# Performance work log

Measured on AMD Instinct MI355X. Metric: run time of the kernel, lower is better.

Reference implementation:

```python
import jax, jax.numpy as jnp
import numpy as np

N_NODES = 100000
IN_CH = 128
HID = 256
EMB = 128
N_EDGES_GRAPH = 1000000
N_PAIRS = 500000
BN_EPS = 1e-5


def setup_inputs() -> dict:
    key = jax.random.key(0)
    ks = jax.random.split(key, 20)
    glorot = lambda k, fi, fo: jax.random.normal(k, (fi, fo), jnp.float32) * (1.0 / np.sqrt(fi))
    pair_dim = EMB * 4 + 2  # 514
    return {
        "x": jax.random.normal(ks[0], (N_NODES, IN_CH), jnp.float32),
        "edge_index": jax.random.randint(ks[1], (2, N_EDGES_GRAPH), 0, N_NODES, jnp.int64),
        "edge_pairs": jax.random.randint(ks[2], (N_PAIRS, 2), 0, N_NODES, jnp.int64),
        # normalizer buffers
        "x_mean": jnp.zeros((IN_CH,), jnp.float32),
        "x_std": jnp.ones((IN_CH,), jnp.float32),
        # log-degree buffer (as after set_degree)
        "log_degree": jax.random.uniform(ks[3], (N_NODES,), jnp.float32) * 5.0,
        # encoder: Linear(in,hid) -> BN(hid) -> ReLU -> Dropout -> Linear(hid,emb) -> ReLU
        "W1": glorot(ks[4], IN_CH, HID), "b1": jnp.zeros((HID,), jnp.float32),
        "bn_gamma": jnp.ones((HID,), jnp.float32), "bn_beta": jnp.zeros((HID,), jnp.float32),
        "bn_mean": jnp.zeros((HID,), jnp.float32), "bn_var": jnp.ones((HID,), jnp.float32),
        "W2": glorot(ks[5], HID, EMB), "b2": jnp.zeros((EMB,), jnp.float32),
        # scorer: Linear(514,256) -> ReLU -> Dropout -> Linear(256,128) -> ReLU -> Linear(128,1)
        "SW1": glorot(ks[6], pair_dim, HID), "Sb1": jnp.zeros((HID,), jnp.float32),
        "SW2": glorot(ks[7], HID, HID // 2), "Sb2": jnp.zeros((HID // 2,), jnp.float32),
        "SW3": glorot(ks[8], HID // 2, 1), "Sb3": jnp.zeros((1,), jnp.float32),
    }


def reference(x, edge_index, edge_pairs, x_mean, x_std, log_degree,
              W1, b1, bn_gamma, bn_beta, bn_mean, bn_var, W2, b2,
              SW1, Sb1, SW2, Sb2, SW3, Sb3):
    # ---- encode ----
    xf = jnp.nan_to_num(x, nan=0.0, posinf=0.0, neginf=0.0)
    xf = jnp.clip((xf - x_mean) / x_std, -10.0, 10.0)
    h = xf @ W1 + b1                                    # [N, HID]
    h = (h - bn_mean) * jax.lax.rsqrt(bn_var + BN_EPS) * bn_gamma + bn_beta  # BN (eval)
    h = jax.nn.relu(h)                                  # dropout = identity (eval)
    z = jax.nn.relu(h @ W2 + b2)                        # [N, EMB]
    # ---- score_from_embeddings ----
    si = edge_pairs[:, 0]
    di = edge_pairs[:, 1]
    src = z[si]                                         # [E, EMB]
    dst = z[di]
    deg_pair = jnp.stack([log_degree[si], log_degree[di]], axis=1)  # [E, 2]
    pair = jnp.concatenate([src, dst, src * dst, jnp.abs(src - dst), deg_pair], axis=1)  # [E, 4*EMB+2]
    s = jax.nn.relu(pair @ SW1 + Sb1)
    s = jax.nn.relu(s @ SW2 + Sb2)
    logits = (s @ SW3 + Sb3).reshape(-1)                # [E]
    return jnp.nan_to_num(logits, nan=0.0, posinf=20.0, neginf=-20.0)
```

## Files before the change

kernel.cpp:

```cpp
#include <hip/hip_runtime.h>
#include <hip/hip_bf16.h>
#include <math.h>

typedef unsigned short u16;
typedef __attribute__((ext_vector_type(8))) short bf16x8;
typedef __attribute__((ext_vector_type(8))) unsigned short u16x8;
typedef __attribute__((ext_vector_type(4))) float f32x4;
typedef __attribute__((ext_vector_type(4))) unsigned u32x4;
typedef __attribute__((ext_vector_type(2))) unsigned u32x2;

#define N_NODES 100000
#define IN_CH 128
#define HID 256
#define EMB 128
#define N_PAIRS 500000
#define BN_EPS 1e-5f

#define PBM 64

__device__ __forceinline__ u16 f2bf(float f) {
    unsigned u = __builtin_bit_cast(unsigned, f);
    unsigned r = u + 0x7FFFu + ((u >> 16) & 1u);
    return (u16)(r >> 16);
}
__device__ __forceinline__ float bf2f(u16 h) {
    unsigned u = ((unsigned)h) << 16;
    return __builtin_bit_cast(float, u);
}
__device__ __forceinline__ unsigned pk2(float a, float b) {
    __hip_bfloat162 h = __float22bfloat162_rn(make_float2(a, b));
    unsigned u;
    __builtin_memcpy(&u, &h, sizeof(u));
    return u;
}
__device__ __forceinline__ float lo16f(unsigned u) { return __builtin_bit_cast(float, u << 16); }
__device__ __forceinline__ float hi16f(unsigned u) { return __builtin_bit_cast(float, u & 0xffff0000u); }

__device__ __forceinline__ void store8(u16* buf, int base, const float* v) {
    u32x4 hv;
    #pragma unroll
    for (int q = 0; q < 4; ++q) hv[q] = pk2(v[2 * q], v[2 * q + 1]);
    *reinterpret_cast<u32x4*>(&buf[base]) = hv;
}

__global__ __launch_bounds__(256) void prep_weights(
    const float* __restrict__ SW1, const float* __restrict__ SW2,
    const float* __restrict__ W1,  const float* __restrict__ W2,
    u16* __restrict__ w1h, u16* __restrict__ w2h,
    u16* __restrict__ w1nh, u16* __restrict__ w1nl,
    u16* __restrict__ w2nh, u16* __restrict__ w2nl)
{
    const int tid = blockIdx.x * 256 + threadIdx.x;
    if (tid < 131072) {
        const int j = tid & 7, l = (tid >> 3) & 63, ks = (tid >> 9) & 15, mt = tid >> 13;
        const int n = mt * 16 + (l & 15);
        const int k = ks * 32 + ((l >> 4) << 3) + j;
        w1h[tid] = f2bf(SW1[(size_t)k * HID + n]);
    } else if (tid < 163840) {
        const int t2 = tid - 131072;
        const int j = t2 & 7, l = (t2 >> 3) & 63, ks = (t2 >> 9) & 7, mt = t2 >> 12;
        const int n = mt * 16 + (l & 15);
        const int k = ks * 32 + ((l >> 4) << 3) + j;
        w2h[t2] = f2bf(SW2[(size_t)k * (HID / 2) + n]);
    } else if (tid < 196608) {
        const int t3 = tid - 163840;
        const int j = t3 & 7, l = (t3 >> 3) & 63, ks = (t3 >> 9) & 3, mt = t3 >> 11;
        const int n = mt * 16 + (l & 15);
        const int k = ks * 32 + ((l >> 4) << 3) + j;
        const float v = W1[(size_t)k * HID + n];
        const u16 h = f2bf(v);
        w1nh[t3] = h;
        w1nl[t3] = f2bf(v - bf2f(h));
    } else if (tid < 229376) {
        const int t4 = tid - 196608;
        const int j = t4 & 7, l = (t4 >> 3) & 63, ks = (t4 >> 9) & 7, mt = t4 >> 12;
        const int n = mt * 16 + (l & 15);
        const int k = ks * 32 + ((l >> 4) << 3) + j;
        const float v = W2[(size_t)k * EMB + n];
        const u16 h = f2bf(v);
        w2nh[t4] = h;
        w2nl[t4] = f2bf(v - bf2f(h));
    }
}

__global__ __launch_bounds__(256) void node_mfma_kernel(
    const float* __restrict__ x,
    const float* __restrict__ x_mean, const float* __restrict__ x_std,
    const float* __restrict__ b1,
    const float* __restrict__ bn_gamma, const float* __restrict__ bn_beta,
    const float* __restrict__ bn_mean,  const float* __restrict__ bn_var,
    const float* __restrict__ b2,
    const u16* __restrict__ w1nh, const u16* __restrict__ w1nl,
    const u16* __restrict__ w2nh, const u16* __restrict__ w2nl,
    u16* __restrict__ z)
{
    __shared__ __align__(16) u16 XF[8192];
    __shared__ __align__(16) u16 HF[16384];

    const int t   = threadIdx.x;
    const int w   = t >> 6;
    const int l   = t & 63;
    const int l15 = l & 15;
    const int l4  = l >> 4;
    const int n0  = blockIdx.x * 64;
    const int nd  = (n0 + l < N_NODES) ? (n0 + l) : (N_NODES - 1);

    {
        const float* xp = x + (size_t)nd * IN_CH + w * 32;
        float v[32];
        #pragma unroll
        for (int q = 0; q < 8; ++q)
            *reinterpret_cast<float4*>(&v[q * 4]) = *reinterpret_cast<const float4*>(xp + q * 4);
        #pragma unroll
        for (int q = 0; q < 8; ++q) {
            float4 m4 = *reinterpret_cast<const float4*>(x_mean + w * 32 + q * 4);
            float4 s4 = *reinterpret_cast<const float4*>(x_std  + w * 32 + q * 4);
            float mm[4] = {m4.x, m4.y, m4.z, m4.w};
            float ss[4] = {s4.x, s4.y, s4.z, s4.w};
            #pragma unroll
            for (int e = 0; e < 4; ++e) {
                float val = v[q * 4 + e];
                if (!isfinite(val)) val = 0.0f;
                val = (val - mm[e]) / ss[e];
                v[q * 4 + e] = fminf(fmaxf(val, -10.0f), 10.0f);
            }
        }
        #pragma unroll
        for (int q = 0; q < 4; ++q) {
            const int base = (w * 4 + l4) * 512 + (l15 + 16 * q) * 8;
            store8(XF, base, &v[q * 8]);
        }
    }
    __syncthreads();

    f32x4 acc[4][4];
    #pragma unroll
    for (int m = 0; m < 4; ++m)
        #pragma unroll
        for (int nt = 0; nt < 4; ++nt) acc[m][nt] = (f32x4){0.f, 0.f, 0.f, 0.f};

    #pragma unroll
    for (int sl = 0; sl < 4; ++sl) {
        bf16x8 wh[4], wl[4];
        #pragma unroll
        for (int m = 0; m < 4; ++m) {
            const size_t bo = ((size_t)((w * 4 + m) * 4 + sl) * 64 + l) * 8;
            wh[m] = *reinterpret_cast<const bf16x8*>(&w1nh[bo]);
            wl[m] = *reinterpret_cast<const bf16x8*>(&w1nl[bo]);
        }
        bf16x8 fh[4];
        #pragma unroll
        for (int nt = 0; nt < 4; ++nt)
            fh[nt] = *reinterpret_cast<const bf16x8*>(&XF[(sl * 4 + nt) * 512 + l * 8]);
        __builtin_amdgcn_s_setprio(1);
        #pragma unroll
        for (int m = 0; m < 4; ++m)
            #pragma unroll
            for (int nt = 0; nt < 4; ++nt)
                acc[m][nt] = __builtin_amdgcn_mfma_f32_16x16x32_bf16(wh[m], fh[nt], acc[m][nt], 0, 0, 0);
        #pragma unroll
        for (int m = 0; m < 4; ++m)
            #pragma unroll
            for (int nt = 0; nt < 4; ++nt)
                acc[m][nt] = __builtin_amdgcn_mfma_f32_16x16x32_bf16(wl[m], fh[nt], acc[m][nt], 0, 0, 0);
        __builtin_amdgcn_s_setprio(0);
    }

    #pragma unroll
    for (int m = 0; m < 4; ++m) {
        const int mt = w * 4 + m;
        const int nb = mt * 16 + l4 * 4;
        float4 b1v = *reinterpret_cast<const float4*>(b1 + nb);
        float4 gv  = *reinterpret_cast<const float4*>(bn_gamma + nb);
        float4 bev = *reinterpret_cast<const float4*>(bn_beta + nb);
        float4 mev = *reinterpret_cast<const float4*>(bn_mean + nb);
        float4 vav = *reinterpret_cast<const float4*>(bn_var + nb);
        float scale[4], shift[4];
        float bb[4] = {b1v.x, b1v.y, b1v.z, b1v.w};
        float gg[4] = {gv.x, gv.y, gv.z, gv.w};
        float be[4] = {bev.x, bev.y, bev.z, bev.w};
        float me[4] = {mev.x, mev.y, mev.z, mev.w};
        float va[4] = {vav.x, vav.y, vav.z, vav.w};
        #pragma unroll
        for (int r = 0; r < 4; ++r) {
            scale[r] = gg[r] * rsqrtf(va[r] + BN_EPS);
            shift[r] = (bb[r] - me[r]) * scale[r] + be[r];
        }
        #pragma unroll
        for (int nt = 0; nt < 4; ++nt) {
            float v[4];
            #pragma unroll
            for (int r = 0; r < 4; ++r)
                v[r] = fmaxf(fmaf(acc[m][nt][r], scale[r], shift[r]), 0.0f);
            u32x2 hv;
            hv[0] = pk2(v[0], v[1]);
            hv[1] = pk2(v[2], v[3]);
            const int base = ((mt >> 1) * 4 + nt) * 512
                           + (l15 + 16 * ((mt & 1) * 2 + (l4 >> 1))) * 8
                           + (l4 & 1) * 4;
            *reinterpret_cast<u32x2*>(&HF[base]) = hv;
        }
    }
    __syncthreads();

    f32x4 acc2[2][4];
    #pragma unroll
    for (int m2 = 0; m2 < 2; ++m2)
        #pragma unroll
        for (int nt = 0; nt < 4; ++nt) acc2[m2][nt] = (f32x4){0.f, 0.f, 0.f, 0.f};

    #pragma unroll
    for (int ks2 = 0; ks2 < 8; ++ks2) {
        bf16x8 wh2[2], wl2[2];
        #pragma unroll
        for (int m2 = 0; m2 < 2; ++m2) {
            const size_t bo = ((size_t)((w * 2 + m2) * 8 + ks2) * 64 + l) * 8;
            wh2[m2] = *reinterpret_cast<const bf16x8*>(&w2nh[bo]);
            wl2[m2] = *reinterpret_cast<const bf16x8*>(&w2nl[bo]);
        }
        bf16x8 fh[4];
        #pragma unroll
        for (int nt = 0; nt < 4; ++nt)
            fh[nt] = *reinterpret_cast<const bf16x8*>(&HF[(ks2 * 4 + nt) * 512 + l * 8]);
        __builtin_amdgcn_s_setprio(1);
        #pragma unroll
        for (int m2 = 0; m2 < 2; ++m2)
            #pragma unroll
            for (int nt = 0; nt < 4; ++nt)
                acc2[m2][nt] = __builtin_amdgcn_mfma_f32_16x16x32_bf16(wh2[m2], fh[nt], acc2[m2][nt], 0, 0, 0);
        #pragma unroll
        for (int m2 = 0; m2 < 2; ++m2)
            #pragma unroll
            for (int nt = 0; nt < 4; ++nt)
                acc2[m2][nt] = __builtin_amdgcn_mfma_f32_16x16x32_bf16(wl2[m2], fh[nt], acc2[m2][nt], 0, 0, 0);
        __builtin_amdgcn_s_setprio(0);
    }

    #pragma unroll
    for (int m2 = 0; m2 < 2; ++m2) {
        const int nb2 = (w * 2 + m2) * 16 + l4 * 4;
        float4 b2v = *reinterpret_cast<const float4*>(b2 + nb2);
        float bb[4] = {b2v.x, b2v.y, b2v.z, b2v.w};
        #pragma unroll
        for (int nt = 0; nt < 4; ++nt) {
            const int node = n0 + nt * 16 + l15;
            if (node < N_NODES) {
                float v0 = fmaxf(acc2[m2][nt][0] + bb[0], 0.0f);
                float v1 = fmaxf(acc2[m2][nt][1] + bb[1], 0.0f);
                float v2 = fmaxf(acc2[m2][nt][2] + bb[2], 0.0f);
                float v3 = fmaxf(acc2[m2][nt][3] + bb[3], 0.0f);
                u32x2 hv;
                hv[0] = pk2(v0, v1);
                hv[1] = pk2(v2, v3);
                *reinterpret_cast<u32x2*>(z + (size_t)node * EMB + nb2) = hv;
            }
        }
    }
}

__global__ __launch_bounds__(256) void pair_mfma_kernel(
    const u16* __restrict__ z,
    const int* __restrict__ pairs,
    const float* __restrict__ logdeg,
    const u16* __restrict__ w1h,
    const u16* __restrict__ w2h,
    const float* __restrict__ SW1, const float* __restrict__ Sb1,
    const float* __restrict__ Sb2,
    const float* __restrict__ SW3, const float* __restrict__ Sb3,
    float* __restrict__ out)
{
    __shared__ __align__(16) u16 Abuf[8192];
    __shared__ __align__(16) u16 Bbuf[8192];
    __shared__ float red[4][4][16];

    const int t   = threadIdx.x;
    const int w   = t >> 6;
    const int l   = t & 63;
    const int l15 = l & 15;
    const int l4  = l >> 4;
    const int p0  = blockIdx.x * PBM;

    const int qb  = (w & 1) * 2;
    const int bS0 = (((w >> 1)) * 4 + l4) * 512 + (l15 + 16 * (qb + 0)) * 8;
    const int bS1 = (((w >> 1)) * 4 + l4) * 512 + (l15 + 16 * (qb + 1)) * 8;
    const int bD0 = ((2 + (w >> 1)) * 4 + l4) * 512 + (l15 + 16 * (qb + 0)) * 8;
    const int bD1 = ((2 + (w >> 1)) * 4 + l4) * 512 + (l15 + 16 * (qb + 1)) * 8;

    const int gp  = (p0 + l < N_PAIRS) ? (p0 + l) : (N_PAIRS - 1);
    const int gsi = pairs[(size_t)gp * 2 + 0];
    const int gdi = pairs[(size_t)gp * 2 + 1];

    const u16* zs0 = z + (size_t)gsi * EMB + w * 16;
    const u16* zd0 = z + (size_t)gdi * EMB + w * 16;
    u16x8 s00 = *reinterpret_cast<const u16x8*>(zs0);
    u16x8 s01 = *reinterpret_cast<const u16x8*>(zs0 + 8);
    u16x8 d00 = *reinterpret_cast<const u16x8*>(zd0);
    u16x8 d01 = *reinterpret_cast<const u16x8*>(zd0 + 8);
    u16x8 s10 = *reinterpret_cast<const u16x8*>(zs0 + 64);
    u16x8 s11 = *reinterpret_cast<const u16x8*>(zs0 + 72);
    u16x8 d10 = *reinterpret_cast<const u16x8*>(zd0 + 64);
    u16x8 d11 = *reinterpret_cast<const u16x8*>(zd0 + 72);

    *reinterpret_cast<u16x8*>(&Abuf[bS0]) = s00;
    *reinterpret_cast<u16x8*>(&Abuf[bS1]) = s01;
    *reinterpret_cast<u16x8*>(&Abuf[bD0]) = d00;
    *reinterpret_cast<u16x8*>(&Abuf[bD1]) = d01;

    float ldS[4], ldD[4];
    #pragma unroll
    for (int nt = 0; nt < 4; ++nt) {
        const int pidx = (p0 + nt * 16 + l15 < N_PAIRS) ? (p0 + nt * 16 + l15) : (N_PAIRS - 1);
        ldS[nt] = logdeg[pairs[(size_t)pidx * 2 + 0]];
        ldD[nt] = logdeg[pairs[(size_t)pidx * 2 + 1]];
    }

    __syncthreads();

    f32x4 acc[4][4];
    #pragma unroll
    for (int m = 0; m < 4; ++m)
        #pragma unroll
        for (int nt = 0; nt < 4; ++nt) acc[m][nt] = (f32x4){0.f, 0.f, 0.f, 0.f};

    auto run_pass = [&](const u16* buf, int k0, int k1, int k2, int k3) {
        const int ksg[4] = {k0, k1, k2, k3};
        bf16x8 wh[2][4];
        #pragma unroll
        for (int m = 0; m < 4; ++m) {
            const size_t bo = ((size_t)((w * 4 + m) * 16 + ksg[0]) * 64 + l) * 8;
            wh[0][m] = *reinterpret_cast<const bf16x8*>(&w1h[bo]);
        }
        #pragma unroll
        for (int sl = 0; sl < 4; ++sl) {
            const int cur = sl & 1;
            if (sl < 3) {
                #pragma unroll
                for (int m = 0; m < 4; ++m) {
                    const size_t bo = ((size_t)((w * 4 + m) * 16 + ksg[sl + 1]) * 64 + l) * 8;
                    wh[cur ^ 1][m] = *reinterpret_cast<const bf16x8*>(&w1h[bo]);
                }
            }
            #pragma unroll
            for (int nh = 0; nh < 2; ++nh) {
                bf16x8 fh[2];
                #pragma unroll
                for (int e = 0; e < 2; ++e)
                    fh[e] = *reinterpret_cast<const bf16x8*>(&buf[(sl * 4 + nh * 2 + e) * 512 + l * 8]);
                __builtin_amdgcn_s_setprio(1);
                #pragma unroll
                for (int m = 0; m < 4; ++m)
                    #pragma unroll
                    for (int e = 0; e < 2; ++e)
                        acc[m][nh * 2 + e] = __builtin_amdgcn_mfma_f32_16x16x32_bf16(wh[cur][m], fh[e], acc[m][nh * 2 + e], 0, 0, 0);
                __builtin_amdgcn_s_setprio(0);
            }
        }
    };

    auto rebuildR = [&](u16x8 sa, u16x8 sb, u16x8 da, u16x8 db, float* pv, float* av) {
        #pragma unroll
        for (int qq = 0; qq < 8; ++qq) {
            const float s = bf2f(sa[qq]);
            const float d = bf2f(da[qq]);
            pv[qq] = s * d;
            av[qq] = fabsf(s - d);
        }
        #pragma unroll
        for (int qq = 0; qq < 8; ++qq) {
            const float s = bf2f(sb[qq]);
            const float d = bf2f(db[qq]);
            pv[8 + qq] = s * d;
            av[8 + qq] = fabsf(s - d);
        }
    };

    run_pass(Abuf, 0, 1, 4, 5);
    {
        float pv[16], av[16];
        rebuildR(s00, s01, d00, d01, pv, av);
        store8(Bbuf, bS0, pv + 0);
        store8(Bbuf, bS1, pv + 8);
        store8(Bbuf, bD0, av + 0);
        store8(Bbuf, bD1, av + 8);
    }
    __syncthreads();

    *reinterpret_cast<u16x8*>(&Abuf[bS0]) = s10;
    *reinterpret_cast<u16x8*>(&Abuf[bS1]) = s11;
    *reinterpret_cast<u16x8*>(&Abuf[bD0]) = d10;
    *reinterpret_cast<u16x8*>(&Abuf[bD1]) = d11;
    run_pass(Bbuf, 8, 9, 12, 13);
    __syncthreads();

    run_pass(Abuf, 2, 3, 6, 7);
    {
        float pv[16], av[16];
        rebuildR(s10, s11, d10, d11, pv, av);
        store8(Bbuf, bS0, pv + 0);
        store8(Bbuf, bS1, pv + 8);
        store8(Bbuf, bD0, av + 0);
        store8(Bbuf, bD1, av + 8);
    }
    __syncthreads();

    run_pass(Bbuf, 10, 11, 14, 15);

    f32x4 acc2[2][4];
    #pragma unroll
    for (int m2 = 0; m2 < 2; ++m2)
        #pragma unroll
        for (int nt = 0; nt < 4; ++nt) acc2[m2][nt] = (f32x4){0.f, 0.f, 0.f, 0.f};

    auto epi1 = [&](u16* buf, int g) {
        #pragma unroll
        for (int mm = 0; mm < 2; ++mm) {
            const int m  = 2 * g + mm;
            const int mt = w * 4 + m;
            const int nb = mt * 16 + l4 * 4;
            float sb[4], wa[4], wb[4];
            *reinterpret_cast<float4*>(sb) = *reinterpret_cast<const float4*>(&Sb1[nb]);
            *reinterpret_cast<float4*>(wa) = *reinterpret_cast<const float4*>(&SW1[(size_t)512 * HID + nb]);
            *reinterpret_cast<float4*>(wb) = *reinterpret_cast<const float4*>(&SW1[(size_t)513 * HID + nb]);
            #pragma unroll
            for (int nt = 0; nt < 4; ++nt) {
                float v[4];
                #pragma unroll
                for (int r = 0; r < 4; ++r) {
                    float x0 = acc[m][nt][r] + sb[r];
                    x0 = fmaf(ldS[nt], wa[r], x0);
                    x0 = fmaf(ldD[nt], wb[r], x0);
                    v[r] = fmaxf(x0, 0.0f);
                }
                u32x2 hv;
                hv[0] = pk2(v[0], v[1]);
                hv[1] = pk2(v[2], v[3]);
                const int base = (w * 4 + nt) * 512
                               + (l15 + 16 * ((m & 1) * 2 + (l4 >> 1))) * 8
                               + (l4 & 1) * 4;
                *reinterpret_cast<u32x2*>(&buf[base]) = hv;
            }
        }
    };

    auto mfma2 = [&](const u16* buf, int g) {
        #pragma unroll
        for (int cs = 0; cs < 4; ++cs) {
            const int ks2 = cs * 2 + g;
            bf16x8 wh2[2];
            #pragma unroll
            for (int m2 = 0; m2 < 2; ++m2) {
                const size_t bo = ((size_t)((w * 2 + m2) * 8 + ks2) * 64 + l) * 8;
                wh2[m2] = *reinterpret_cast<const bf16x8*>(&w2h[bo]);
            }
            #pragma unroll
            for (int nh = 0; nh < 2; ++nh) {
                bf16x8 fh[2];
                #pragma unroll
                for (int e = 0; e < 2; ++e)
                    fh[e] = *reinterpret_cast<const bf16x8*>(&buf[(cs * 4 + nh * 2 + e) * 512 + l * 8]);
                __builtin_amdgcn_s_setprio(1);
                #pragma unroll
                for (int m2 = 0; m2 < 2; ++m2)
                    #pragma unroll
                    for (int e = 0; e < 2; ++e)
                        acc2[m2][nh * 2 + e] = __builtin_amdgcn_mfma_f32_16x16x32_bf16(wh2[m2], fh[e], acc2[m2][nh * 2 + e], 0, 0, 0);
                __builtin_amdgcn_s_setprio(0);
            }
        }
    };

    epi1(Abuf, 0);
    __syncthreads();
    epi1(Bbuf, 1);
    mfma2(Abuf, 0);
    __syncthreads();
    mfma2(Bbuf, 1);

    {
        float part[4] = {0.f, 0.f, 0.f, 0.f};
        #pragma unroll
        for (int m2 = 0; m2 < 2; ++m2) {
            const int nb2 = (w * 2 + m2) * 16 + l4 * 4;
            float sb[4], w3[4];
            *reinterpret_cast<float4*>(sb) = *reinterpret_cast<const float4*>(&Sb2[nb2]);
            *reinterpret_cast<float4*>(w3) = *reinterpret_cast<const float4*>(&SW3[nb2]);
            #pragma unroll
            for (int nt = 0; nt < 4; ++nt)
                #pragma unroll
                for (int r = 0; r < 4; ++r)
                    part[nt] = fmaf(fmaxf(acc2[m2][nt][r] + sb[r], 0.0f), w3[r], part[nt]);
        }
        #pragma unroll
        for (int nt = 0; nt < 4; ++nt) {
            part[nt] += __shfl_xor(part[nt], 16);
            part[nt] += __shfl_xor(part[nt], 32);
        }
        if (l < 16) {
            #pragma unroll
            for (int nt = 0; nt < 4; ++nt) red[w][nt][l15] = part[nt];
        }
    }
    __syncthreads();

    if (t < 64) {
        const int nt = t >> 4, pp = t & 15;
        float v = red[0][nt][pp] + red[1][nt][pp] + red[2][nt][pp] + red[3][nt][pp] + Sb3[0];
        if (isnan(v)) v = 0.0f;
        else if (isinf(v)) v = (v > 0.0f) ? 20.0f : -20.0f;
        const int pidx = p0 + nt * 16 + pp;
        if (pidx < N_PAIRS) out[pidx] = v;
    }
}

extern "C" void kernel_launch(void* const* d_in, const int* in_sizes, int n_in,
                              void* d_out, int out_size, void* d_ws, size_t ws_size,
                              hipStream_t stream)
{
    const float* x        = (const float*)d_in[0];
    const int*   pairs    = (const int*)d_in[2];
    const float* x_mean   = (const float*)d_in[3];
    const float* x_std    = (const float*)d_in[4];
    const float* logdeg   = (const float*)d_in[5];
    const float* W1       = (const float*)d_in[6];
    const float* b1       = (const float*)d_in[7];
    const float* bn_gamma = (const float*)d_in[8];
    const float* bn_beta  = (const float*)d_in[9];
    const float* bn_mean  = (const float*)d_in[10];
    const float* bn_var   = (const float*)d_in[11];
    const float* W2       = (const float*)d_in[12];
    const float* b2       = (const float*)d_in[13];
    const float* SW1      = (const float*)d_in[14];
    const float* Sb1      = (const float*)d_in[15];
    const float* SW2      = (const float*)d_in[16];
    const float* Sb2      = (const float*)d_in[17];
    const float* SW3      = (const float*)d_in[18];
    const float* Sb3      = (const float*)d_in[19];

    float* outp = (float*)d_out;

    char* wsb = (char*)d_ws;
    u16* zbuf = (u16*)wsb;
    u16* w1h  = (u16*)(wsb + 25600000);
    u16* w2h  = (u16*)(wsb + 25862144);
    u16* w1nh = (u16*)(wsb + 25927680);
    u16* w1nl = (u16*)(wsb + 25993216);
    u16* w2nh = (u16*)(wsb + 26058752);
    u16* w2nl = (u16*)(wsb + 26124288);

    prep_weights<<<896, 256, 0, stream>>>(SW1, SW2, W1, W2,
                                          w1h, w2h,
                                          w1nh, w1nl, w2nh, w2nl);

    node_mfma_kernel<<<(N_NODES + 63) / 64, 256, 0, stream>>>(
        x, x_mean, x_std, b1, bn_gamma, bn_beta, bn_mean, bn_var, b2,
        w1nh, w1nl, w2nh, w2nl, zbuf);

    pair_mfma_kernel<<<(N_PAIRS + PBM - 1) / PBM, 256, 0, stream>>>(
        zbuf, pairs, logdeg, w1h, w2h, SW1, Sb1, Sb2, SW3, Sb3, outp);
}
```

Before: 256.3 us.

## Split pair kernel work across eight waves per block instead of four

The pair-scoring kernel now runs with 512 threads (8 waves) per 64-pair block. Each wave owns half as many output tiles in both MLP layers, so per-wave accumulators and weight registers shrink, and the LDS staging layout, epilogue ownership and final reduction are remapped for eight waves. The aim is lower register pressure and more latency hiding per CU. In exchange, barriers now synchronize more waves and each wave has less independent MFMA work to interleave.

```diff
diff --git a/kernel.cpp b/kernel.cpp
--- a/kernel.cpp
+++ b/kernel.cpp
@@ -33,8 +33,6 @@
     __builtin_memcpy(&u, &h, sizeof(u));
     return u;
 }
-__device__ __forceinline__ float lo16f(unsigned u) { return __builtin_bit_cast(float, u << 16); }
-__device__ __forceinline__ float hi16f(unsigned u) { return __builtin_bit_cast(float, u & 0xffff0000u); }
 
 __device__ __forceinline__ void store8(u16* buf, int base, const float* v) {
     u32x4 hv;
@@ -258,7 +256,7 @@
     }
 }
 
-__global__ __launch_bounds__(256) void pair_mfma_kernel(
+__global__ __launch_bounds__(512) void pair_mfma_kernel(
     const u16* __restrict__ z,
     const int* __restrict__ pairs,
     const float* __restrict__ logdeg,
@@ -271,7 +269,7 @@
 {
     __shared__ __align__(16) u16 Abuf[8192];
     __shared__ __align__(16) u16 Bbuf[8192];
-    __shared__ float red[4][4][16];
+    __shared__ float red[8][4][16];
 
     const int t   = threadIdx.x;
     const int w   = t >> 6;
@@ -280,31 +278,22 @@
     const int l4  = l >> 4;
     const int p0  = blockIdx.x * PBM;
 
-    const int qb  = (w & 1) * 2;
-    const int bS0 = (((w >> 1)) * 4 + l4) * 512 + (l15 + 16 * (qb + 0)) * 8;
-    const int bS1 = (((w >> 1)) * 4 + l4) * 512 + (l15 + 16 * (qb + 1)) * 8;
-    const int bD0 = ((2 + (w >> 1)) * 4 + l4) * 512 + (l15 + 16 * (qb + 0)) * 8;
-    const int bD1 = ((2 + (w >> 1)) * 4 + l4) * 512 + (l15 + 16 * (qb + 1)) * 8;
+    const int baseS = (((w >> 2)) * 4 + l4) * 512 + (l15 + 16 * (w & 3)) * 8;
+    const int baseD = ((2 + (w >> 2)) * 4 + l4) * 512 + (l15 + 16 * (w & 3)) * 8;
 
     const int gp  = (p0 + l < N_PAIRS) ? (p0 + l) : (N_PAIRS - 1);
     const int gsi = pairs[(size_t)gp * 2 + 0];
     const int gdi = pairs[(size_t)gp * 2 + 1];
 
-    const u16* zs0 = z + (size_t)gsi * EMB + w * 16;
-    const u16* zd0 = z + (size_t)gdi * EMB + w * 16;
-    u16x8 s00 = *reinterpret_cast<const u16x8*>(zs0);
-    u16x8 s01 = *reinterpret_cast<const u16x8*>(zs0 + 8);
-    u16x8 d00 = *reinterpret_cast<const u16x8*>(zd0);
-    u16x8 d01 = *reinterpret_cast<const u16x8*>(zd0 + 8);
-    u16x8 s10 = *reinterpret_cast<const u16x8*>(zs0 + 64);
-    u16x8 s11 = *reinterpret_cast<const u16x8*>(zs0 + 72);
-    u16x8 d10 = *reinterpret_cast<const u16x8*>(zd0 + 64);
-    u16x8 d11 = *reinterpret_cast<const u16x8*>(zd0 + 72);
-
-    *reinterpret_cast<u16x8*>(&Abuf[bS0]) = s00;
-    *reinterpret_cast<u16x8*>(&Abuf[bS1]) = s01;
-    *reinterpret_cast<u16x8*>(&Abuf[bD0]) = d00;
-    *reinterpret_cast<u16x8*>(&Abuf[bD1]) = d01;
+    const u16* zs0 = z + (size_t)gsi * EMB + w * 8;
+    const u16* zd0 = z + (size_t)gdi * EMB + w * 8;
+    u16x8 s0 = *reinterpret_cast<const u16x8*>(zs0);
+    u16x8 d0 = *reinterpret_cast<const u16x8*>(zd0);
+    u16x8 s1 = *reinterpret_cast<const u16x8*>(zs0 + 64);
+    u16x8 d1 = *reinterpret_cast<const u16x8*>(zd0 + 64);
+
+    *reinterpret_cast<u16x8*>(&Abuf[baseS]) = s0;
+    *reinterpret_cast<u16x8*>(&Abuf[baseD]) = d0;
 
     float ldS[4], ldD[4];
     #pragma unroll
@@ -316,18 +305,18 @@
 
     __syncthreads();
 
-    f32x4 acc[4][4];
-    #pragma unroll
-    for (int m = 0; m < 4; ++m)
+    f32x4 acc[2][4];
+    #pragma unroll
+    for (int m = 0; m < 2; ++m)
         #pragma unroll
         for (int nt = 0; nt < 4; ++nt) acc[m][nt] = (f32x4){0.f, 0.f, 0.f, 0.f};
 
     auto run_pass = [&](const u16* buf, int k0, int k1, int k2, int k3) {
         const int ksg[4] = {k0, k1, k2, k3};
-        bf16x8 wh[2][4];
-        #pragma unroll
-        for (int m = 0; m < 4; ++m) {
-            const size_t bo = ((size_t)((w * 4 + m) * 16 + ksg[0]) * 64 + l) * 8;
+        bf16x8 wh[2][2];
+        #pragma unroll
+        for (int m = 0; m < 2; ++m) {
+            const size_t bo = ((size_t)((w * 2 + m) * 16 + ksg[0]) * 64 + l) * 8;
             wh[0][m] = *reinterpret_cast<const bf16x8*>(&w1h[bo]);
         }
         #pragma unroll
@@ -335,8 +324,8 @@
             const int cur = sl & 1;
             if (sl < 3) {
                 #pragma unroll
-                for (int m = 0; m < 4; ++m) {
-                    const size_t bo = ((size_t)((w * 4 + m) * 16 + ksg[sl + 1]) * 64 + l) * 8;
+                for (int m = 0; m < 2; ++m) {
+                    const size_t bo = ((size_t)((w * 2 + m) * 16 + ksg[sl + 1]) * 64 + l) * 8;
                     wh[cur ^ 1][m] = *reinterpret_cast<const bf16x8*>(&w1h[bo]);
                 }
             }
@@ -348,7 +337,7 @@
                     fh[e] = *reinterpret_cast<const bf16x8*>(&buf[(sl * 4 + nh * 2 + e) * 512 + l * 8]);
                 __builtin_amdgcn_s_setprio(1);
                 #pragma unroll
-                for (int m = 0; m < 4; ++m)
+                for (int m = 0; m < 2; ++m)
                     #pragma unroll
                     for (int e = 0; e < 2; ++e)
                         acc[m][nh * 2 + e] = __builtin_amdgcn_mfma_f32_16x16x32_bf16(wh[cur][m], fh[e], acc[m][nh * 2 + e], 0, 0, 0);
@@ -357,7 +346,7 @@
         }
     };
 
-    auto rebuildR = [&](u16x8 sa, u16x8 sb, u16x8 da, u16x8 db, float* pv, float* av) {
+    auto rebuildR = [&](u16x8 sa, u16x8 da, float* pv, float* av) {
         #pragma unroll
         for (int qq = 0; qq < 8; ++qq) {
             const float s = bf2f(sa[qq]);
@@ -365,57 +354,41 @@
             pv[qq] = s * d;
             av[qq] = fabsf(s - d);
         }
-        #pragma unroll
-        for (int qq = 0; qq < 8; ++qq) {
-            const float s = bf2f(sb[qq]);
-            const float d = bf2f(db[qq]);
-            pv[8 + qq] = s * d;
-            av[8 + qq] = fabsf(s - d);
-        }
     };
 
     run_pass(Abuf, 0, 1, 4, 5);
     {
-        float pv[16], av[16];
-        rebuildR(s00, s01, d00, d01, pv, av);
-        store8(Bbuf, bS0, pv + 0);
-        store8(Bbuf, bS1, pv + 8);
-        store8(Bbuf, bD0, av + 0);
-        store8(Bbuf, bD1, av + 8);
-    }
-    __syncthreads();
-
-    *reinterpret_cast<u16x8*>(&Abuf[bS0]) = s10;
-    *reinterpret_cast<u16x8*>(&Abuf[bS1]) = s11;
-    *reinterpret_cast<u16x8*>(&Abuf[bD0]) = d10;
-    *reinterpret_cast<u16x8*>(&Abuf[bD1]) = d11;
+        float pv[8], av[8];
+        rebuildR(s0, d0, pv, av);
+        store8(Bbuf, baseS, pv);
+        store8(Bbuf, baseD, av);
+    }
+    __syncthreads();
+
+    *reinterpret_cast<u16x8*>(&Abuf[baseS]) = s1;
+    *reinterpret_cast<u16x8*>(&Abuf[baseD]) = d1;
     run_pass(Bbuf, 8, 9, 12, 13);
     __syncthreads();
 
     run_pass(Abuf, 2, 3, 6, 7);
     {
-        float pv[16], av[16];
-        rebuildR(s10, s11, d10, d11, pv, av);
-        store8(Bbuf, bS0, pv + 0);
-        store8(Bbuf, bS1, pv + 8);
-        store8(Bbuf, bD0, av + 0);
-        store8(Bbuf, bD1, av + 8);
+        float pv[8], av[8];
+        rebuildR(s1, d1, pv, av);
+        store8(Bbuf, baseS, pv);
+        store8(Bbuf, baseD, av);
     }
     __syncthreads();
 
     run_pass(Bbuf, 10, 11, 14, 15);
 
-    f32x4 acc2[2][4];
-    #pragma unroll
-    for (int m2 = 0; m2 < 2; ++m2)
-        #pragma unroll
-        for (int nt = 0; nt < 4; ++nt) acc2[m2][nt] = (f32x4){0.f, 0.f, 0.f, 0.f};
-
-    auto epi1 = [&](u16* buf, int g) {
-        #pragma unroll
-        for (int mm = 0; mm < 2; ++mm) {
-            const int m  = 2 * g + mm;
-            const int mt = w * 4 + m;
+    f32x4 acc2[4];
+    #pragma unroll
+    for (int nt = 0; nt < 4; ++nt) acc2[nt] = (f32x4){0.f, 0.f, 0.f, 0.f};
+
+    auto epi1 = [&](u16* buf) {
+        #pragma unroll
+        for (int m = 0; m < 2; ++m) {
+            const int mt = w * 2 + m;
             const int nb = mt * 16 + l4 * 4;
             float sb[4], wa[4], wb[4];
             *reinterpret_cast<float4*>(sb) = *reinterpret_cast<const float4*>(&Sb1[nb]);
@@ -434,8 +407,8 @@
                 u32x2 hv;
                 hv[0] = pk2(v[0], v[1]);
                 hv[1] = pk2(v[2], v[3]);
-                const int base = (w * 4 + nt) * 512
-                               + (l15 + 16 * ((m & 1) * 2 + (l4 >> 1))) * 8
+                const int base = ((w >> 1) * 4 + nt) * 512
+                               + (l15 + 16 * (m * 2 + (l4 >> 1))) * 8
                                + (l4 & 1) * 4;
                 *reinterpret_cast<u32x2*>(&buf[base]) = hv;
             }
@@ -446,12 +419,8 @@
         #pragma unroll
         for (int cs = 0; cs < 4; ++cs) {
             const int ks2 = cs * 2 + g;
-            bf16x8 wh2[2];
-            #pragma unroll
-            for (int m2 = 0; m2 < 2; ++m2) {
-                const size_t bo = ((size_t)((w * 2 + m2) * 8 + ks2) * 64 + l) * 8;
-                wh2[m2] = *reinterpret_cast<const bf16x8*>(&w2h[bo]);
-            }
+            const size_t bo = ((size_t)(w * 8 + ks2) * 64 + l) * 8;
+            bf16x8 wh2 = *reinterpret_cast<const bf16x8*>(&w2h[bo]);
             #pragma unroll
             for (int nh = 0; nh < 2; ++nh) {
                 bf16x8 fh[2];
@@ -460,36 +429,31 @@
                     fh[e] = *reinterpret_cast<const bf16x8*>(&buf[(cs * 4 + nh * 2 + e) * 512 + l * 8]);
                 __builtin_amdgcn_s_setprio(1);
                 #pragma unroll
-                for (int m2 = 0; m2 < 2; ++m2)
-                    #pragma unroll
-                    for (int e = 0; e < 2; ++e)
-                        acc2[m2][nh * 2 + e] = __builtin_amdgcn_mfma_f32_16x16x32_bf16(wh2[m2], fh[e], acc2[m2][nh * 2 + e], 0, 0, 0);
+                for (int e = 0; e < 2; ++e)
+                    acc2[nh * 2 + e] = __builtin_amdgcn_mfma_f32_16x16x32_bf16(wh2, fh[e], acc2[nh * 2 + e], 0, 0, 0);
                 __builtin_amdgcn_s_setprio(0);
             }
         }
     };
 
-    epi1(Abuf, 0);
-    __syncthreads();
-    epi1(Bbuf, 1);
+    if ((w & 1) == 0) epi1(Abuf);
+    __syncthreads();
+    if ((w & 1) == 1) epi1(Bbuf);
     mfma2(Abuf, 0);
     __syncthreads();
     mfma2(Bbuf, 1);
 
     {
         float part[4] = {0.f, 0.f, 0.f, 0.f};
-        #pragma unroll
-        for (int m2 = 0; m2 < 2; ++m2) {
-            const int nb2 = (w * 2 + m2) * 16 + l4 * 4;
-            float sb[4], w3[4];
-            *reinterpret_cast<float4*>(sb) = *reinterpret_cast<const float4*>(&Sb2[nb2]);
-            *reinterpret_cast<float4*>(w3) = *reinterpret_cast<const float4*>(&SW3[nb2]);
-            #pragma unroll
-            for (int nt = 0; nt < 4; ++nt)
-                #pragma unroll
-                for (int r = 0; r < 4; ++r)
-                    part[nt] = fmaf(fmaxf(acc2[m2][nt][r] + sb[r], 0.0f), w3[r], part[nt]);
-        }
+        const int nb2 = w * 16 + l4 * 4;
+        float sb[4], w3[4];
+        *reinterpret_cast<float4*>(sb) = *reinterpret_cast<const float4*>(&Sb2[nb2]);
+        *reinterpret_cast<float4*>(w3) = *reinterpret_cast<const float4*>(&SW3[nb2]);
+        #pragma unroll
+        for (int nt = 0; nt < 4; ++nt)
+            #pragma unroll
+            for (int r = 0; r < 4; ++r)
+                part[nt] = fmaf(fmaxf(acc2[nt][r] + sb[r], 0.0f), w3[r], part[nt]);
         #pragma unroll
         for (int nt = 0; nt < 4; ++nt) {
             part[nt] += __shfl_xor(part[nt], 16);
@@ -504,7 +468,9 @@
 
     if (t < 64) {
         const int nt = t >> 4, pp = t & 15;
-        float v = red[0][nt][pp] + red[1][nt][pp] + red[2][nt][pp] + red[3][nt][pp] + Sb3[0];
+        float v = Sb3[0];
+        #pragma unroll
+        for (int ww = 0; ww < 8; ++ww) v += red[ww][nt][pp];
         if (isnan(v)) v = 0.0f;
         else if (isinf(v)) v = (v > 0.0f) ? 20.0f : -20.0f;
         const int pidx = p0 + nt * 16 + pp;
@@ -555,6 +521,6 @@
         x, x_mean, x_std, b1, bn_gamma, bn_beta, bn_mean, bn_var, b2,
         w1nh, w1nl, w2nh, w2nl, zbuf);
 
-    pair_mfma_kernel<<<(N_PAIRS + PBM - 1) / PBM, 256, 0, stream>>>(
+    pair_mfma_kernel<<<(N_PAIRS + PBM - 1) / PBM, 512, 0, stream>>>(
         zbuf, pairs, logdeg, w1h, w2h, SW1, Sb1, Sb2, SW3, Sb3, outp);
 }
```

New measurement: 274.6 us. 7.2% more time.
